# Performance work log

Hardware: AMD Instinct MI355X
Metric: run time of the kernel (lower is better)

Reference implementation:

```python
import jax, jax.numpy as jnp
import numpy as np

H = 4            # attention heads
N = 50000        # num nodes
E = 800000       # num edges
IN, HID, OUT = 256, 32, 32
NEG_SLOPE = 0.2  # DGL GATConv default leaky_relu slope


def setup_inputs() -> dict:
    key = jax.random.key(0)
    ks = jax.random.split(key, 16)
    x = jax.random.normal(ks[0], (N, IN), jnp.float32)
    src = jax.random.randint(ks[1], (E,), 0, N, dtype=jnp.int32)
    dst = jax.random.randint(ks[2], (E,), 0, N, dtype=jnp.int32)

    def lin(k, a, b):
        return jax.random.normal(k, (a, b), jnp.float32) * (1.0 / np.sqrt(a))

    def attn(k, d):
        return jax.random.normal(k, (H, d), jnp.float32) * 0.1

    HW = H * HID
    return {
        "x": x, "src": src, "dst": dst,
        "W1": lin(ks[3], IN, HW), "al1": attn(ks[4], HID), "ar1": attn(ks[5], HID), "b1": jnp.zeros((H, HID), jnp.float32),
        "W2": lin(ks[6], HW, HW), "al2": attn(ks[7], HID), "ar2": attn(ks[8], HID), "b2": jnp.zeros((H, HID), jnp.float32),
        "W3": lin(ks[9], HW, H * OUT), "al3": attn(ks[10], OUT), "ar3": attn(ks[11], OUT), "b3": jnp.zeros((H, OUT), jnp.float32),
    }


def gat_layer(x, W, al, ar, b, src, dst, act):
    # x: [N, F_in]; W: [F_in, H*D]; al/ar/b: [H, D]
    n = x.shape[0]
    d = al.shape[1]
    h = (x @ W).reshape(n, H, d)                         # [N, H, D]
    el = jnp.sum(h * al, axis=-1)                        # [N, H]
    er = jnp.sum(h * ar, axis=-1)                        # [N, H]
    e = jax.nn.leaky_relu(el[src] + er[dst], NEG_SLOPE)  # [E, H] edge scores
    # segment softmax over incoming edges of each dst node
    m = jax.ops.segment_max(e, dst, num_segments=n)      # [N, H]
    m = jnp.where(jnp.isfinite(m), m, 0.0)               # empty segments -> -inf
    ex = jnp.exp(e - m[dst])                             # [E, H]
    s = jax.ops.segment_sum(ex, dst, num_segments=n)     # [N, H]
    alpha = ex / s[dst]                                  # [E, H]
    out = jax.ops.segment_sum(h[src] * alpha[:, :, None], dst, num_segments=n)  # [N, H, D]
    out = out + b
    return act(out) if act is not None else out


def reference(x, src, dst, W1, al1, ar1, b1, W2, al2, ar2, b2, W3, al3, ar3, b3):
    h = gat_layer(x, W1, al1, ar1, b1, src, dst, jax.nn.relu).reshape(N, -1)   # flatten heads
    h = gat_layer(h, W2, al2, ar2, b2, src, dst, jax.nn.elu).reshape(N, -1)    # flatten heads
    h = gat_layer(h, W3, al3, ar3, b3, src, dst, None).mean(axis=1)            # mean over heads
    return h
```

## Files before the change

### kernel.cpp

```cpp
#include <hip/hip_runtime.h>
#include <hip/hip_bf16.h>
#include <hip/hip_fp16.h>
#include <stdint.h>

#define NNODES 50000
#define NEDGES 800000
#define HEADS 4
#define DSTRIDE 64

#define GEMM_GRID ((NNODES + 127) / 128)
#define B2_GROUPS 8
#define B2_PER_GROUP 256
#define NODES_PER_GROUP (NNODES / B2_GROUPS)

typedef __attribute__((ext_vector_type(8))) short bf16x8;
typedef __attribute__((ext_vector_type(4))) float f32x4;

union frag_u { uint32_t u[4]; bf16x8 v; uint4 q; };

__device__ __forceinline__ float lrelu(float x) { return x > 0.f ? x : 0.2f * x; }

__device__ __forceinline__ uint32_t pack_bf16(float a, float b) {
  __hip_bfloat162 t{__float2bfloat16(a), __float2bfloat16(b)};
  return *reinterpret_cast<uint32_t*>(&t);
}

__device__ __forceinline__ void split8(const float4& x0, const float4& x1,
                                       frag_u& hi, frag_u& lo) {
  float f[8] = {x0.x, x0.y, x0.z, x0.w, x1.x, x1.y, x1.z, x1.w};
#pragma unroll
  for (int p = 0; p < 4; ++p) {
    uint32_t ua = __float_as_uint(f[2 * p]);
    uint32_t ub = __float_as_uint(f[2 * p + 1]);
    hi.u[p] = (ua >> 16) | (ub & 0xffff0000u);
    float ra = f[2 * p] - __uint_as_float(ua & 0xffff0000u);
    float rb = f[2 * p + 1] - __uint_as_float(ub & 0xffff0000u);
    lo.u[p] = (__float_as_uint(ra) >> 16) | (__float_as_uint(rb) & 0xffff0000u);
  }
}

__global__ __launch_bounds__(256) void k_build2(const int* __restrict__ src,
                                                const int* __restrict__ dst,
                                                int* __restrict__ cnt,
                                                int* __restrict__ esrc) {
  int g = blockIdx.x & (B2_GROUPS - 1);
  int sub = blockIdx.x >> 3;
  int lo = g * NODES_PER_GROUP, hi = lo + NODES_PER_GROUP;
  const int tstride = B2_PER_GROUP * 256 * 4;
  for (int e = (sub * 256 + threadIdx.x) * 4; e < NEDGES; e += tstride) {
    int4 d4 = *(const int4*)&dst[e];
    if (d4.x >= lo && d4.x < hi) {
      int r = atomicAdd(&cnt[d4.x], 1);
      if (r < DSTRIDE) esrc[(size_t)d4.x * DSTRIDE + r] = src[e];
    }
    if (d4.y >= lo && d4.y < hi) {
      int r = atomicAdd(&cnt[d4.y], 1);
      if (r < DSTRIDE) esrc[(size_t)d4.y * DSTRIDE + r] = src[e + 1];
    }
    if (d4.z >= lo && d4.z < hi) {
      int r = atomicAdd(&cnt[d4.z], 1);
      if (r < DSTRIDE) esrc[(size_t)d4.z * DSTRIDE + r] = src[e + 2];
    }
    if (d4.w >= lo && d4.w < hi) {
      int r = atomicAdd(&cnt[d4.w], 1);
      if (r < DSTRIDE) esrc[(size_t)d4.w * DSTRIDE + r] = src[e + 3];
    }
  }
}

__device__ __forceinline__ void splitw_one(const float* __restrict__ W, int t_local,
                                           uint4* __restrict__ WPh, uint4* __restrict__ WPl) {
  int lane = t_local & 63;
  int ct = (t_local >> 6) & 7;
  int ks = t_local >> 9;
  int lg = lane >> 4, lm = lane & 15;
  int n = ct * 16 + lm;
  frag_u hi, lo;
#pragma unroll
  for (int p = 0; p < 4; ++p) {
    float a = W[(size_t)(ks * 32 + lg * 8 + 2 * p) * 128 + n];
    float b = W[(size_t)(ks * 32 + lg * 8 + 2 * p + 1) * 128 + n];
    uint32_t ua = __float_as_uint(a), ub = __float_as_uint(b);
    hi.u[p] = (ua >> 16) | (ub & 0xffff0000u);
    float ra = a - __uint_as_float(ua & 0xffff0000u);
    float rb = b - __uint_as_float(ub & 0xffff0000u);
    lo.u[p] = (__float_as_uint(ra) >> 16) | (__float_as_uint(rb) & 0xffff0000u);
  }
  WPh[t_local] = hi.q;
  WPl[t_local] = lo.q;
}

__global__ void k_splitw_all(const float* __restrict__ W1, const float* __restrict__ W2,
                             const float* __restrict__ W3,
                             uint4* __restrict__ WPh1, uint4* __restrict__ WPl1,
                             uint4* __restrict__ WPh2, uint4* __restrict__ WPl2,
                             uint4* __restrict__ WPh3, uint4* __restrict__ WPl3,
                             int* __restrict__ cnt) {
  int t = blockIdx.x * blockDim.x + threadIdx.x;
  for (int i = t; i < NNODES; i += 32 * 256) cnt[i] = 0;
  int ks = t >> 9;
  if (ks < 8)        splitw_one(W1, t,            WPh1, WPl1);
  else if (ks < 12)  splitw_one(W2, t - 8 * 512,  WPh2, WPl2);
  else if (ks < 16)  splitw_one(W3, t - 12 * 512, WPh3, WPl3);
}

template <int K, int XBF>
__global__ __launch_bounds__(256) void k_gemm_mfma(
    const void* __restrict__ Xv, const uint4* __restrict__ WPh,
    const uint4* __restrict__ WPl, const float* __restrict__ al,
    const float* __restrict__ ar, uint32_t* __restrict__ Hb,
    float* __restrict__ el, float* __restrict__ er, int nrows) {
  __shared__ uint4 lph[512];
  __shared__ uint4 lpl[512];
  const int tid = threadIdx.x;
  const int wv = tid >> 6;
  const int lane = tid & 63;
  const int lm = lane & 15;
  const int lg = lane >> 4;
  const int rbase = blockIdx.x * 128 + wv * 32;

  int grow0 = rbase + lm;
  int grow1 = rbase + 16 + lm;
  int lrow0 = min(grow0, nrows - 1);
  int lrow1 = min(grow1, nrows - 1);

  const float* xp0 = nullptr;
  const float* xp1 = nullptr;
  const uint32_t* xq0 = nullptr;
  const uint32_t* xq1 = nullptr;
  if (XBF) {
    xq0 = (const uint32_t*)Xv + (size_t)lrow0 * 64 + lg * 4;
    xq1 = (const uint32_t*)Xv + (size_t)lrow1 * 64 + lg * 4;
  } else {
    xp0 = (const float*)Xv + (size_t)lrow0 * K + lg * 8;
    xp1 = (const float*)Xv + (size_t)lrow1 * K + lg * 8;
  }

  f32x4 acc[2][8];
#pragma unroll
  for (int rt = 0; rt < 2; ++rt)
#pragma unroll
    for (int ct = 0; ct < 8; ++ct) acc[rt][ct] = f32x4{0.f, 0.f, 0.f, 0.f};

  for (int ks = 0; ks < K / 32; ++ks) {
    frag_u xh0, xl0, xh1, xl1;
    if (XBF) {
      xh0.q = *(const uint4*)(xq0 + ks * 16);
      xh1.q = *(const uint4*)(xq1 + ks * 16);
    } else {
      float4 a0 = *(const float4*)(xp0 + ks * 32);
      float4 a1 = *(const float4*)(xp0 + ks * 32 + 4);
      float4 b0 = *(const float4*)(xp1 + ks * 32);
      float4 b1 = *(const float4*)(xp1 + ks * 32 + 4);
      split8(a0, a1, xh0, xl0);
      split8(b0, b1, xh1, xl1);
    }
    lph[tid]       = WPh[(size_t)ks * 512 + tid];
    lph[tid + 256] = WPh[(size_t)ks * 512 + 256 + tid];
    lpl[tid]       = WPl[(size_t)ks * 512 + tid];
    lpl[tid + 256] = WPl[(size_t)ks * 512 + 256 + tid];
    __syncthreads();
#pragma unroll
    for (int ct = 0; ct < 8; ++ct) {
      frag_u bh, bl;
      bh.q = lph[ct * 64 + lane];
      bl.q = lpl[ct * 64 + lane];
      if (XBF) {
        acc[0][ct] = __builtin_amdgcn_mfma_f32_16x16x32_bf16(bh.v, xh0.v, acc[0][ct], 0, 0, 0);
        acc[0][ct] = __builtin_amdgcn_mfma_f32_16x16x32_bf16(bl.v, xh0.v, acc[0][ct], 0, 0, 0);
        acc[1][ct] = __builtin_amdgcn_mfma_f32_16x16x32_bf16(bh.v, xh1.v, acc[1][ct], 0, 0, 0);
        acc[1][ct] = __builtin_amdgcn_mfma_f32_16x16x32_bf16(bl.v, xh1.v, acc[1][ct], 0, 0, 0);
      } else {
        acc[0][ct] = __builtin_amdgcn_mfma_f32_16x16x32_bf16(bh.v, xh0.v, acc[0][ct], 0, 0, 0);
        acc[0][ct] = __builtin_amdgcn_mfma_f32_16x16x32_bf16(bl.v, xh0.v, acc[0][ct], 0, 0, 0);
        acc[0][ct] = __builtin_amdgcn_mfma_f32_16x16x32_bf16(bh.v, xl0.v, acc[0][ct], 0, 0, 0);
        acc[1][ct] = __builtin_amdgcn_mfma_f32_16x16x32_bf16(bh.v, xh1.v, acc[1][ct], 0, 0, 0);
        acc[1][ct] = __builtin_amdgcn_mfma_f32_16x16x32_bf16(bl.v, xh1.v, acc[1][ct], 0, 0, 0);
        acc[1][ct] = __builtin_amdgcn_mfma_f32_16x16x32_bf16(bh.v, xl1.v, acc[1][ct], 0, 0, 0);
      }
    }
    __syncthreads();
  }

#pragma unroll
  for (int rt = 0; rt < 2; ++rt) {
    int grow = rt ? grow1 : grow0;
    float pe[4] = {0.f, 0.f, 0.f, 0.f};
    float pr[4] = {0.f, 0.f, 0.f, 0.f};
#pragma unroll
    for (int ct = 0; ct < 8; ++ct) {
      int h = ct >> 1;
      int dc = (ct & 1) * 16 + lg * 4;
      float4 a4 = *(const float4*)&al[h * 32 + dc];
      float4 r4 = *(const float4*)&ar[h * 32 + dc];
      f32x4 c = acc[rt][ct];
      pe[h] += c[0] * a4.x + c[1] * a4.y + c[2] * a4.z + c[3] * a4.w;
      pr[h] += c[0] * r4.x + c[1] * r4.y + c[2] * r4.z + c[3] * r4.w;
    }
#pragma unroll
    for (int i = 0; i < 4; ++i) {
      pe[i] += __shfl_xor(pe[i], 16); pe[i] += __shfl_xor(pe[i], 32);
      pr[i] += __shfl_xor(pr[i], 16); pr[i] += __shfl_xor(pr[i], 32);
    }
    if (grow < nrows) {
#pragma unroll
      for (int ct = 0; ct < 8; ++ct) {
        f32x4 c = acc[rt][ct];
        uint2 st{pack_bf16(c[0], c[1]), pack_bf16(c[2], c[3])};
        *(uint2*)&Hb[(size_t)grow * 64 + ct * 8 + lg * 2] = st;
      }
      if (lg == 0) {
        *(float4*)&el[(size_t)grow * 4] = float4{pe[0], pe[1], pe[2], pe[3]};
        *(float4*)&er[(size_t)grow * 4] = float4{pr[0], pr[1], pr[2], pr[3]};
      }
    }
  }
}

template <int MODE>
__global__ __launch_bounds__(256) void k_agg(const uint32_t* __restrict__ Hb,
                                             const float* __restrict__ el,
                                             const float* __restrict__ er,
                                             const int* __restrict__ deg_,
                                             const int* __restrict__ esrc,
                                             const float* __restrict__ B,
                                             void* __restrict__ outp) {
  int gt = blockIdx.x * blockDim.x + threadIdx.x;
  int v = gt >> 6;
  int lane = gt & 63;
  if (v >= NNODES) return;
  int deg = min(deg_[v], DSTRIDE);
  int h = lane >> 4;
  int e16 = lane & 15;
  float erh = er[(size_t)v * 4 + h];
  const int vbase = v * DSTRIDE;

  float den = 0.f, acc0 = 0.f, acc1 = 0.f;
  for (int base = 0; base < deg; base += 16) {
    uint32_t pk = 0;
    if (base + e16 < deg) {
      int u = esrc[vbase + base + e16];
      float ex1 = __expf(lrelu(el[(size_t)u * 4 + h] + erh));
      den += ex1;
      pk = ((uint32_t)u << 16) | (uint32_t)__half_as_ushort(__float2half(ex1));
    }
    uint32_t hw[16];
    float w[16];
#pragma unroll
    for (int j = 0; j < 16; ++j) {
      int srcl = (lane & 48) | j;
      uint32_t pkj = __shfl(pk, srcl);
      w[j] = __half2float(__ushort_as_half((unsigned short)(pkj & 0xffffu)));
      hw[j] = Hb[(size_t)(pkj >> 16) * 64 + lane];
    }
#pragma unroll
    for (int j = 0; j < 16; ++j) {
      acc0 += w[j] * __uint_as_float(hw[j] << 16);
      acc1 += w[j] * __uint_as_float(hw[j] & 0xffff0000u);
    }
  }
#pragma unroll
  for (int s = 1; s < 16; s <<= 1) den += __shfl_xor(den, s);
  float inv = den > 0.f ? 1.f / den : 0.f;

  int d = (2 * lane) & 31;
  float v0 = acc0 * inv + B[h * 32 + d];
  float v1 = acc1 * inv + B[h * 32 + d + 1];

  if (MODE == 0) {
    ((uint32_t*)outp)[(size_t)v * 64 + lane] = pack_bf16(fmaxf(v0, 0.f), fmaxf(v1, 0.f));
  } else if (MODE == 1) {
    float a0 = v0 > 0.f ? v0 : expm1f(v0);
    float a1 = v1 > 0.f ? v1 : expm1f(v1);
    ((uint32_t*)outp)[(size_t)v * 64 + lane] = pack_bf16(a0, a1);
  } else {
    float t0 = v0, t1 = v1;
    t0 += __shfl_xor(t0, 16); t0 += __shfl_xor(t0, 32);
    t1 += __shfl_xor(t1, 16); t1 += __shfl_xor(t1, 32);
    if (lane < 16) {
      float2 o{t0 * 0.25f, t1 * 0.25f};
      *(float2*)((float*)outp + (size_t)v * 32 + 2 * lane) = o;
    }
  }
}

extern "C" void kernel_launch(void* const* d_in, const int* in_sizes, int n_in,
                              void* d_out, int out_size, void* d_ws, size_t ws_size,
                              hipStream_t stream) {
  const float* x   = (const float*)d_in[0];
  const int* src   = (const int*)d_in[1];
  const int* dst   = (const int*)d_in[2];
  const float* W1  = (const float*)d_in[3];
  const float* al1 = (const float*)d_in[4];
  const float* ar1 = (const float*)d_in[5];
  const float* b1  = (const float*)d_in[6];
  const float* W2  = (const float*)d_in[7];
  const float* al2 = (const float*)d_in[8];
  const float* ar2 = (const float*)d_in[9];
  const float* b2  = (const float*)d_in[10];
  const float* W3  = (const float*)d_in[11];
  const float* al3 = (const float*)d_in[12];
  const float* ar3 = (const float*)d_in[13];
  const float* b3  = (const float*)d_in[14];

  uint8_t* p = (uint8_t*)d_ws;
  auto alloc = [&](size_t bytes) {
    uint8_t* r = p;
    p += (bytes + 255) & ~(size_t)255;
    return r;
  };
  uint32_t* Hb    = (uint32_t*)alloc((size_t)NNODES * 64 * 4);
  uint32_t* Ab    = (uint32_t*)alloc((size_t)NNODES * 64 * 4);
  float* el       = (float*)alloc((size_t)NNODES * 4 * 4);
  float* er       = (float*)alloc((size_t)NNODES * 4 * 4);
  int* cnt        = (int*)alloc((size_t)NNODES * 4);
  int* esrc       = (int*)alloc((size_t)NNODES * DSTRIDE * 4);
  uint4* WPh1     = (uint4*)alloc((size_t)256 * 16 * 16);
  uint4* WPl1     = (uint4*)alloc((size_t)256 * 16 * 16);
  uint4* WPh2     = (uint4*)alloc((size_t)128 * 16 * 16);
  uint4* WPl2     = (uint4*)alloc((size_t)128 * 16 * 16);
  uint4* WPh3     = (uint4*)alloc((size_t)128 * 16 * 16);
  uint4* WPl3     = (uint4*)alloc((size_t)128 * 16 * 16);

  k_splitw_all<<<32, 256, 0, stream>>>(W1, W2, W3, WPh1, WPl1, WPh2, WPl2,
                                       WPh3, WPl3, cnt);
  k_build2<<<B2_GROUPS * B2_PER_GROUP, 256, 0, stream>>>(src, dst, cnt, esrc);

  const int agg_grid = (NNODES * 64 + 255) / 256;

  k_gemm_mfma<256, 0><<<GEMM_GRID, 256, 0, stream>>>(x, WPh1, WPl1, al1, ar1, Hb, el, er, NNODES);
  k_agg<0><<<agg_grid, 256, 0, stream>>>(Hb, el, er, cnt, esrc, b1, Ab);

  k_gemm_mfma<128, 1><<<GEMM_GRID, 256, 0, stream>>>(Ab, WPh2, WPl2, al2, ar2, Hb, el, er, NNODES);
  k_agg<1><<<agg_grid, 256, 0, stream>>>(Hb, el, er, cnt, esrc, b2, Ab);

  k_gemm_mfma<128, 1><<<GEMM_GRID, 256, 0, stream>>>(Ab, WPh3, WPl3, al3, ar3, Hb, el, er, NNODES);
  k_agg<2><<<agg_grid, 256, 0, stream>>>(Hb, el, er, cnt, esrc, b3, d_out);
}
```

Before: 215.5 us.

## Store edge sources as 16-bit, prefetch next edge chunk, widen build loads

Shrinks the per-destination source index table from 32-bit to 16-bit, which halves the bytes written by the build and read by each of the three aggregation passes. The aggregation loop now computes the next 16-edge chunk's scores and packed indices before accumulating the current chunk, so the gathers overlap with the FMA work. The build kernel also has each thread handle 8 edges per iteration. Node ids reach 49999, which fits in 16 bits (the old code already packed u<<16 into 32 bits). Prefetching adds register pressure.

```diff
diff --git a/kernel.cpp b/kernel.cpp
--- a/kernel.cpp
+++ b/kernel.cpp
@@ -42,28 +42,22 @@
 __global__ __launch_bounds__(256) void k_build2(const int* __restrict__ src,
                                                 const int* __restrict__ dst,
                                                 int* __restrict__ cnt,
-                                                int* __restrict__ esrc) {
+                                                unsigned short* __restrict__ esrc) {
   int g = blockIdx.x & (B2_GROUPS - 1);
   int sub = blockIdx.x >> 3;
   int lo = g * NODES_PER_GROUP, hi = lo + NODES_PER_GROUP;
-  const int tstride = B2_PER_GROUP * 256 * 4;
-  for (int e = (sub * 256 + threadIdx.x) * 4; e < NEDGES; e += tstride) {
-    int4 d4 = *(const int4*)&dst[e];
-    if (d4.x >= lo && d4.x < hi) {
-      int r = atomicAdd(&cnt[d4.x], 1);
-      if (r < DSTRIDE) esrc[(size_t)d4.x * DSTRIDE + r] = src[e];
-    }
-    if (d4.y >= lo && d4.y < hi) {
-      int r = atomicAdd(&cnt[d4.y], 1);
-      if (r < DSTRIDE) esrc[(size_t)d4.y * DSTRIDE + r] = src[e + 1];
-    }
-    if (d4.z >= lo && d4.z < hi) {
-      int r = atomicAdd(&cnt[d4.z], 1);
-      if (r < DSTRIDE) esrc[(size_t)d4.z * DSTRIDE + r] = src[e + 2];
-    }
-    if (d4.w >= lo && d4.w < hi) {
-      int r = atomicAdd(&cnt[d4.w], 1);
-      if (r < DSTRIDE) esrc[(size_t)d4.w * DSTRIDE + r] = src[e + 3];
+  const int tstride = B2_PER_GROUP * 256 * 8;
+  for (int e = (sub * 256 + threadIdx.x) * 8; e < NEDGES; e += tstride) {
+    int4 da = *(const int4*)&dst[e];
+    int4 db = *(const int4*)&dst[e + 4];
+#pragma unroll
+    for (int q = 0; q < 8; ++q) {
+      int d = q < 4 ? (q == 0 ? da.x : q == 1 ? da.y : q == 2 ? da.z : da.w)
+                    : (q == 4 ? db.x : q == 5 ? db.y : q == 6 ? db.z : db.w);
+      if (d >= lo && d < hi) {
+        int r = atomicAdd(&cnt[d], 1);
+        if (r < DSTRIDE) esrc[(size_t)d * DSTRIDE + r] = (unsigned short)src[e + q];
+      }
     }
   }
 }
@@ -222,7 +216,7 @@
                                              const float* __restrict__ el,
                                              const float* __restrict__ er,
                                              const int* __restrict__ deg_,
-                                             const int* __restrict__ esrc,
+                                             const unsigned short* __restrict__ esrc,
                                              const float* __restrict__ B,
                                              void* __restrict__ outp) {
   int gt = blockIdx.x * blockDim.x + threadIdx.x;
@@ -236,7 +230,8 @@
   const int vbase = v * DSTRIDE;
 
   float den = 0.f, acc0 = 0.f, acc1 = 0.f;
-  for (int base = 0; base < deg; base += 16) {
+
+  auto prep = [&](int base) -> uint32_t {
     uint32_t pk = 0;
     if (base + e16 < deg) {
       int u = esrc[vbase + base + e16];
@@ -244,6 +239,11 @@
       den += ex1;
       pk = ((uint32_t)u << 16) | (uint32_t)__half_as_ushort(__float2half(ex1));
     }
+    return pk;
+  };
+
+  uint32_t pk = (deg > 0) ? prep(0) : 0;
+  for (int base = 0; base < deg; base += 16) {
     uint32_t hw[16];
     float w[16];
 #pragma unroll
@@ -253,11 +253,14 @@
       w[j] = __half2float(__ushort_as_half((unsigned short)(pkj & 0xffffu)));
       hw[j] = Hb[(size_t)(pkj >> 16) * 64 + lane];
     }
+    uint32_t pk_next = 0;
+    if (base + 16 < deg) pk_next = prep(base + 16);
 #pragma unroll
     for (int j = 0; j < 16; ++j) {
       acc0 += w[j] * __uint_as_float(hw[j] << 16);
       acc1 += w[j] * __uint_as_float(hw[j] & 0xffff0000u);
     }
+    pk = pk_next;
   }
 #pragma unroll
   for (int s = 1; s < 16; s <<= 1) den += __shfl_xor(den, s);
@@ -309,18 +312,18 @@
     p += (bytes + 255) & ~(size_t)255;
     return r;
   };
-  uint32_t* Hb    = (uint32_t*)alloc((size_t)NNODES * 64 * 4);
-  uint32_t* Ab    = (uint32_t*)alloc((size_t)NNODES * 64 * 4);
-  float* el       = (float*)alloc((size_t)NNODES * 4 * 4);
-  float* er       = (float*)alloc((size_t)NNODES * 4 * 4);
-  int* cnt        = (int*)alloc((size_t)NNODES * 4);
-  int* esrc       = (int*)alloc((size_t)NNODES * DSTRIDE * 4);
-  uint4* WPh1     = (uint4*)alloc((size_t)256 * 16 * 16);
-  uint4* WPl1     = (uint4*)alloc((size_t)256 * 16 * 16);
-  uint4* WPh2     = (uint4*)alloc((size_t)128 * 16 * 16);
-  uint4* WPl2     = (uint4*)alloc((size_t)128 * 16 * 16);
-  uint4* WPh3     = (uint4*)alloc((size_t)128 * 16 * 16);
-  uint4* WPl3     = (uint4*)alloc((size_t)128 * 16 * 16);
+  uint32_t* Hb          = (uint32_t*)alloc((size_t)NNODES * 64 * 4);
+  uint32_t* Ab          = (uint32_t*)alloc((size_t)NNODES * 64 * 4);
+  float* el             = (float*)alloc((size_t)NNODES * 4 * 4);
+  float* er             = (float*)alloc((size_t)NNODES * 4 * 4);
+  int* cnt              = (int*)alloc((size_t)NNODES * 4);
+  unsigned short* esrc  = (unsigned short*)alloc((size_t)NNODES * DSTRIDE * 2);
+  uint4* WPh1           = (uint4*)alloc((size_t)256 * 16 * 16);
+  uint4* WPl1           = (uint4*)alloc((size_t)256 * 16 * 16);
+  uint4* WPh2           = (uint4*)alloc((size_t)128 * 16 * 16);
+  uint4* WPl2           = (uint4*)alloc((size_t)128 * 16 * 16);
+  uint4* WPh3           = (uint4*)alloc((size_t)128 * 16 * 16);
+  uint4* WPl3           = (uint4*)alloc((size_t)128 * 16 * 16);
 
   k_splitw_all<<<32, 256, 0, stream>>>(W1, W2, W3, WPh1, WPl1, WPh2, WPl2,
                                        WPh3, WPl3, cnt);
```

New measurement: 226.1 us. 1.05x slower.
